# Kernel optimization log

Measured on AMD Instinct MI355X. Metric: run time of the kernel, lower is better.

## Reference

```python
import jax, jax.numpy as jnp
import numpy as np
from jax import lax

# Dense-equivalent of the spconv net: SubMConv/SparseConv with stride 1 and
# size-preserving padding on a dense input reduce to ordinary conv2d.
# Layer chain: (1->64,k1) PReLU (64->256,k3) PReLU (256->512,k3) PReLU
# (512->256,k3) PReLU (256->64,k3) PReLU (64->1,k3) PReLU, then symmetrize.

CHANS = [(1, 64, 1), (64, 256, 3), (256, 512, 3), (512, 256, 3), (256, 64, 3), (64, 1, 3)]


def _conv(x, w, b, k):
    pad = ((k // 2, k // 2), (k // 2, k // 2))
    y = lax.conv_general_dilated(x, w, window_strides=(1, 1), padding=pad,
                                 dimension_numbers=('NCHW', 'OIHW', 'NCHW'))
    return y + b[None, :, None, None]


def _prelu(x, a):
    return jnp.where(x >= 0, x, a * x)


def setup_inputs() -> dict:
    key = jax.random.key(0)
    keys = jax.random.split(key, 1 + 2 * len(CHANS))
    inp = {'A': jax.random.normal(keys[0], (1, 1, 512, 512), dtype=jnp.float32)}
    for i, (cin, cout, k) in enumerate(CHANS):
        fan_in = cin * k * k
        std = 1.0 / np.sqrt(fan_in)
        inp[f'w{i}'] = jax.random.normal(keys[1 + 2 * i], (cout, cin, k, k), dtype=jnp.float32) * std
        inp[f'b{i}'] = jax.random.normal(keys[2 + 2 * i], (cout,), dtype=jnp.float32) * std
        inp[f'p{i}'] = jnp.full((1,), 0.25, dtype=jnp.float32)  # PReLU default weight
    return inp


def reference(A, w0, b0, p0, w1, b1, p1, w2, b2, p2, w3, b3, p3, w4, b4, p4, w5, b5, p5):
    params = [(w0, b0, p0), (w1, b1, p1), (w2, b2, p2), (w3, b3, p3), (w4, b4, p4), (w5, b5, p5)]
    x = A
    for (w, b, p), (_, _, k) in zip(params, CHANS):
        x = _prelu(_conv(x, w, b, k), p)
    # make_symmetric: average with transpose over the spatial (matrix) dims
    return 0.5 * (x + jnp.swapaxes(x, -1, -2))
```

## Files before the change

kernel.cpp:

```cpp
#include <hip/hip_runtime.h>
#include <hip/hip_bf16.h>
#include <stdint.h>

typedef __bf16 bf16_t;
typedef __bf16 bf16x8 __attribute__((ext_vector_type(8)));
typedef float  f32x4  __attribute__((ext_vector_type(4)));

#define HP 514
#define AS1 __attribute__((address_space(1)))
#define AS3 __attribute__((address_space(3)))

__device__ __forceinline__ bf16_t f2bf(float f) { return (bf16_t)f; }

__global__ void l0_kernel(const float* __restrict__ A, const float* __restrict__ w0,
                          const float* __restrict__ b0, const float* __restrict__ p0,
                          bf16_t* __restrict__ X0)
{
    int idx = blockIdx.x * 256 + threadIdx.x;
    if (idx >= HP * HP * 64) return;
    int c   = idx & 63;
    int pix = idx >> 6;
    int py = pix / HP, px = pix - py * HP;
    float v = 0.f;
    if (py >= 1 && py <= 512 && px >= 1 && px <= 512) {
        float a = A[(py - 1) * 512 + (px - 1)];
        v = fmaf(w0[c], a, b0[c]);
        v = v >= 0.f ? v : p0[0] * v;
    }
    X0[idx] = f2bf(v);
}

__global__ void zero_rows_kernel(bf16_t* __restrict__ buf, int C, int r0, int n)
{
    int idx = blockIdx.x * 256 + threadIdx.x;
    int rowsz = HP * C;
    if (idx >= n * rowsz) return;
    int r = idx / rowsz, j = idx - r * rowsz;
    buf[(size_t)(r0 + r) * rowsz + j] = f2bf(0.f);
}

__global__ void zero_cols_kernel(bf16_t* __restrict__ buf, int C, int R)
{
    int idx = blockIdx.x * 256 + threadIdx.x;
    if (idx >= R * 2 * C) return;
    int r = idx / (2 * C);
    int t = idx - r * 2 * C;
    int col = (t < C) ? 0 : 513;
    int c = t % C;
    buf[((size_t)r * HP + col) * C + c] = f2bf(0.f);
}

__global__ void wtrans_kernel(const float* __restrict__ w, bf16_t* __restrict__ wt,
                              int COUT, int CIN)
{
    int idx = blockIdx.x * 256 + threadIdx.x;
    if (idx >= COUT * CIN * 9) return;
    int G    = COUT / 16;
    int j    = idx & 7;
    int l    = (idx >> 3) & 63;
    int t    = idx >> 9;
    int gabs = t % G;
    int t2   = t / G;
    int tap  = t2 % 9;
    int ci   = t2 / 9;
    int cout = gabs * 16 + (l & 15);
    int cin  = ci * 32 + (l >> 4) * 8 + j;
    wt[idx] = f2bf(w[(cout * CIN + cin) * 9 + tap]);
}

template<int CIN, int COUT, int BN>
__global__ __launch_bounds__(256, 2)
void conv3x3_kernel(const bf16_t* __restrict__ in, const bf16_t* __restrict__ wt,
                    const float* __restrict__ bias, const float* __restrict__ alpha,
                    bf16_t* __restrict__ out,
                    int n_rows, int in_off, int in_alloc, int out_off)
{
    constexpr int G      = COUT / 16;
    constexpr int GPB    = BN / 16;
    constexpr int NT     = BN / 32;
    constexpr int NC     = CIN / 32;
    constexpr int AUNITS = 18 * 10 * 4;
    constexpr int ASLAB  = AUNITS * 8;
    constexpr int BSZ    = BN * 32;
    __shared__ __align__(16) bf16_t As[2 * ASLAB];
    __shared__ __align__(16) bf16_t Bs[2 * BSZ];

    const int tid  = threadIdx.x;
    const int lane = tid & 63;
    const int wave = tid >> 6;
    const int lm   = lane & 15;
    const int quad = lane >> 4;
    const int wave_m = wave >> 1;
    const int wave_n = wave & 1;

    const int x0 = blockIdx.x * 8;
    const int y0 = blockIdx.y * 16;
    const int zb = blockIdx.z;
    const int gb_blk = zb * GPB;

    int a_src[3], a_dst[3];
    #pragma unroll
    for (int it = 0; it < 3; ++it) {
        int u  = it * 256 + tid;
        int uu = u < AUNITS ? u : 0;
        int q = uu & 3, px = (uu >> 2) % 10, r = uu / 40;
        int grow = in_off + y0 + r;
        grow = grow < 0 ? 0 : (grow >= in_alloc ? in_alloc - 1 : grow);
        a_src[it] = (grow * HP + x0 + px) * CIN + q * 8;
        a_dst[it] = (r * 40 + px * 4 + ((q + (px >> 1)) & 3)) * 8;
    }

    const int pxb = lm & 7, pyb = lm >> 3;
    int sw[3];
    #pragma unroll
    for (int dx = 0; dx < 3; ++dx)
        sw[dx] = ((quad + ((pxb + dx) >> 1)) & 3) * 8;
    int addrA0[4];
    #pragma unroll
    for (int mt = 0; mt < 4; ++mt)
        addrA0[mt] = ((wave_m * 8 + mt * 2 + pyb) * 40 + pxb * 4) * 8;

    auto loadA = [&](int cc, bf16x8* s) {
        #pragma unroll
        for (int it = 0; it < 3; ++it)
            if (it * 256 + tid < AUNITS)
                s[it] = *(const bf16x8*)(in + a_src[it] + cc);
    };
    auto writeA = [&](const bf16x8* s, int abuf) {
        bf16_t* d = As + abuf * ASLAB;
        #pragma unroll
        for (int it = 0; it < 3; ++it)
            if (it * 256 + tid < AUNITS)
                *(bf16x8*)(d + a_dst[it]) = s[it];
    };
    auto stageB = [&](int ci9t, int bbuf) {
        #pragma unroll
        for (int k = 0; k < GPB / 4; ++k) {
            int g = wave + k * 4;
            const bf16_t* src = wt + ((size_t)ci9t * G + gb_blk + g) * 512 + lane * 8;
            bf16_t* dst = Bs + bbuf * BSZ + g * 512;
            __builtin_amdgcn_global_load_lds((AS1 void*)src, (AS3 void*)dst, 16, 0, 0);
        }
    };

    f32x4 acc[4][NT] = {};
    bf16x8 areg[3];

    loadA(0, areg);
    writeA(areg, 0);
    stageB(0, 0);
    __syncthreads();

    int ab = 0, bb = 0;
    for (int ci = 0; ci < NC; ++ci) {
        const bool more = (ci + 1 < NC);
        #pragma unroll
        for (int tap = 0; tap < 9; ++tap) {
            if (tap < 8)      stageB(ci * 9 + tap + 1, bb ^ 1);
            else if (more)    stageB((ci + 1) * 9, bb ^ 1);
            if (tap == 0 && more) loadA((ci + 1) * 32, areg);

            const int dy = tap / 3, dx = tap - dy * 3;
            const int shift = (dy * 40 + dx * 4) * 8 + sw[dx];
            bf16x8 a[4], b[NT];
            #pragma unroll
            for (int nt = 0; nt < NT; ++nt)
                b[nt] = *(const bf16x8*)(Bs + bb * BSZ + (wave_n * NT + nt) * 512 + lane * 8);
            #pragma unroll
            for (int mt = 0; mt < 4; ++mt)
                a[mt] = *(const bf16x8*)(As + ab * ASLAB + addrA0[mt] + shift);
            #pragma unroll
            for (int mt = 0; mt < 4; ++mt)
                #pragma unroll
                for (int nt = 0; nt < NT; ++nt)
                    acc[mt][nt] = __builtin_amdgcn_mfma_f32_16x16x32_bf16(
                        a[mt], b[nt], acc[mt][nt], 0, 0, 0);

            if (tap == 8 && more) writeA(areg, ab ^ 1);
            __syncthreads();
            bb ^= 1;
        }
        ab ^= 1;
    }

    const float al = alpha[0];
    #pragma unroll
    for (int nt = 0; nt < NT; ++nt) {
        const int n = zb * BN + wave_n * (BN / 2) + nt * 16 + lm;
        const float bv = bias[n];
        #pragma unroll
        for (int mt = 0; mt < 4; ++mt) {
            f32x4 v = acc[mt][nt];
            #pragma unroll
            for (int r = 0; r < 4; ++r) {
                int m  = wave_m * 64 + mt * 16 + quad * 4 + r;
                int py = m >> 3, px = m & 7;
                int ly = y0 + py;
                if (ly < n_rows) {
                    float f = v[r] + bv;
                    f = f >= 0.f ? f : al * f;
                    out[((size_t)(out_off + ly) * HP + (x0 + px + 1)) * COUT + n] = f2bf(f);
                }
            }
        }
    }
}

__device__ __forceinline__ float conv64_at(const bf16_t* __restrict__ X,
                                           const float* __restrict__ wsh,
                                           int y, int x, float bv)
{
    float acc = bv;
    #pragma unroll
    for (int dy = 0; dy < 3; ++dy) {
        #pragma unroll
        for (int dx = 0; dx < 3; ++dx) {
            const bf16x8* p = (const bf16x8*)(X + ((size_t)(y + dy) * HP + (x + dx)) * 64);
            const float* wf = wsh + (dy * 3 + dx) * 64;
            #pragma unroll
            for (int j = 0; j < 8; ++j) {
                bf16x8 v = p[j];
                #pragma unroll
                for (int k = 0; k < 8; ++k)
                    acc = fmaf((float)v[k], wf[j * 8 + k], acc);
            }
        }
    }
    return acc;
}

__global__ __launch_bounds__(256)
void l5_strip_kernel(const bf16_t* __restrict__ B4, const bf16_t* __restrict__ wt5,
                     const float* __restrict__ b5, const float* __restrict__ p5,
                     float* __restrict__ T, int abs_row0)
{
    __shared__ float wsh[9 * 64];
    for (int i = threadIdx.x; i < 576; i += 256) wsh[i] = (float)wt5[i];
    __syncthreads();
    int idx = blockIdx.x * 256 + threadIdx.x;
    int ly = idx >> 9, x = idx & 511;
    float bv = b5[0], al = p5[0];
    float t = conv64_at(B4, wsh, ly, x, bv);
    t = t >= 0.f ? t : al * t;
    T[(size_t)(abs_row0 + ly) * 512 + x] = t;
}

__global__ void wtrans5_kernel(const float* __restrict__ w, bf16_t* __restrict__ wt)
{
    int idx = blockIdx.x * 256 + threadIdx.x;
    if (idx >= 9 * 64) return;
    int cin = idx % 64, tap = idx / 64;
    wt[idx] = f2bf(w[cin * 9 + tap]);
}

__global__ __launch_bounds__(256)
void sym_kernel(const float* __restrict__ T, float* __restrict__ out)
{
    int idx = blockIdx.x * 256 + threadIdx.x;
    int y = idx >> 9, x = idx & 511;
    out[idx] = 0.5f * (T[idx] + T[x * 512 + y]);
}

extern "C" void kernel_launch(void* const* d_in, const int* in_sizes, int n_in,
                              void* d_out, int out_size, void* d_ws, size_t ws_size,
                              hipStream_t stream)
{
    const float* A = (const float*)d_in[0];
    const float *w[6], *b[6], *p[6];
    for (int i = 0; i < 6; ++i) {
        w[i] = (const float*)d_in[1 + 3 * i];
        b[i] = (const float*)d_in[2 + 3 * i];
        p[i] = (const float*)d_in[3 + 3 * i];
    }

    auto footprint = [](long long S) -> size_t {
        auto al = [](size_t v) { return (v + 255) & ~(size_t)255; };
        size_t t = 0;
        t += al((size_t)HP * HP * 64 * 2);
        t += al((size_t)(S + 8) * HP * 256 * 2);
        t += al((size_t)(S + 6) * HP * 512 * 2);
        t += al((size_t)(S + 2) * HP * 64 * 2);
        t += al((size_t)512 * 512 * 4);
        t += al((size_t)9 * 256 * 64 * 2);
        t += al((size_t)9 * 512 * 256 * 2);
        t += al((size_t)9 * 256 * 512 * 2);
        t += al((size_t)9 * 64 * 256 * 2);
        t += al((size_t)9 * 64 * 2);
        return t;
    };
    const int cand[6] = {512, 256, 128, 64, 32, 16};
    int S = 16;
    for (int i = 0; i < 6; ++i)
        if (footprint(cand[i]) <= ws_size) { S = cand[i]; break; }
    const int nStrips = 512 / S;

    char* ws = (char*)d_ws;
    size_t off = 0;
    auto carve = [&](size_t bytes) -> void* {
        void* r = ws + off;
        off += (bytes + 255) & ~(size_t)255;
        return r;
    };
    bf16_t* X0  = (bf16_t*)carve((size_t)HP * HP * 64 * 2);
    bf16_t* B1  = (bf16_t*)carve((size_t)(S + 8) * HP * 256 * 2);
    bf16_t* B2  = (bf16_t*)carve((size_t)(S + 6) * HP * 512 * 2);
    bf16_t* B4  = (bf16_t*)carve((size_t)(S + 2) * HP * 64 * 2);
    float*  T   = (float*)carve((size_t)512 * 512 * 4);
    bf16_t* wt1 = (bf16_t*)carve((size_t)9 * 256 * 64 * 2);
    bf16_t* wt2 = (bf16_t*)carve((size_t)9 * 512 * 256 * 2);
    bf16_t* wt3 = (bf16_t*)carve((size_t)9 * 256 * 512 * 2);
    bf16_t* wt4 = (bf16_t*)carve((size_t)9 * 64 * 256 * 2);
    bf16_t* wt5 = (bf16_t*)carve((size_t)9 * 64 * 2);
    bf16_t* B3  = B1;

    auto cdiv = [](int a, int bq) { return (a + bq - 1) / bq; };
    auto zrows = [&](bf16_t* buf, int C, int r0, int n) {
        if (n > 0)
            zero_rows_kernel<<<cdiv(n * HP * C, 256), 256, 0, stream>>>(buf, C, r0, n);
    };

    wtrans_kernel<<<cdiv(9 * 256 * 64, 256), 256, 0, stream>>>(w[1], wt1, 256, 64);
    wtrans_kernel<<<cdiv(9 * 512 * 256, 256), 256, 0, stream>>>(w[2], wt2, 512, 256);
    wtrans_kernel<<<cdiv(9 * 256 * 512, 256), 256, 0, stream>>>(w[3], wt3, 256, 512);
    wtrans_kernel<<<cdiv(9 * 64 * 256, 256), 256, 0, stream>>>(w[4], wt4, 64, 256);
    wtrans5_kernel<<<cdiv(9 * 64, 256), 256, 0, stream>>>(w[5], wt5);
    l0_kernel<<<cdiv(HP * HP * 64, 256), 256, 0, stream>>>(A, w[0], b[0], p[0], X0);
    zero_cols_kernel<<<cdiv((S + 8) * 2 * 256, 256), 256, 0, stream>>>(B1, 256, S + 8);
    zero_cols_kernel<<<cdiv((S + 6) * 2 * 512, 256), 256, 0, stream>>>(B2, 512, S + 6);
    zero_cols_kernel<<<cdiv((S + 2) * 2 * 64, 256), 256, 0, stream>>>(B4, 64, S + 2);

    for (int s = 0; s < nStrips; ++s) {
        const int base = S * s;
        int o0[5], nn[5], ooff[5], alloc[5];
        for (int k = 1; k <= 4; ++k) {
            int hk = 5 - k;
            int a0 = base - hk, a1 = base + S + hk;
            int c0 = a0 < 0 ? 0 : a0, c1 = a1 > 512 ? 512 : a1;
            o0[k] = c0; nn[k] = c1 - c0; ooff[k] = c0 - a0; alloc[k] = S + 2 * hk;
        }
        {
            int in_off = o0[1];
            dim3 g(64, cdiv(nn[1], 16), 2);
            conv3x3_kernel<64, 256, 128><<<g, 256, 0, stream>>>(
                X0, wt1, b[1], p[1], B1, nn[1], in_off, 514, ooff[1]);
            zrows(B1, 256, 0, ooff[1]);
            zrows(B1, 256, ooff[1] + nn[1], alloc[1] - ooff[1] - nn[1]);
        }
        {
            int in_off = (o0[2] - 1) - (base - 4);
            dim3 g(64, cdiv(nn[2], 16), 4);
            conv3x3_kernel<256, 512, 128><<<g, 256, 0, stream>>>(
                B1, wt2, b[2], p[2], B2, nn[2], in_off, alloc[1], ooff[2]);
            zrows(B2, 512, 0, ooff[2]);
            zrows(B2, 512, ooff[2] + nn[2], alloc[2] - ooff[2] - nn[2]);
        }
        {
            int in_off = (o0[3] - 1) - (base - 3);
            dim3 g(64, cdiv(nn[3], 16), 2);
            conv3x3_kernel<512, 256, 128><<<g, 256, 0, stream>>>(
                B2, wt3, b[3], p[3], B3, nn[3], in_off, alloc[2], ooff[3]);
            zrows(B3, 256, 0, ooff[3]);
            zrows(B3, 256, ooff[3] + nn[3], alloc[3] - ooff[3] - nn[3]);
        }
        {
            int in_off = (o0[4] - 1) - (base - 2);
            dim3 g(64, cdiv(nn[4], 16), 1);
            conv3x3_kernel<256, 64, 64><<<g, 256, 0, stream>>>(
                B3, wt4, b[4], p[4], B4, nn[4], in_off, alloc[3], ooff[4]);
            zrows(B4, 64, 0, ooff[4]);
            zrows(B4, 64, ooff[4] + nn[4], alloc[4] - ooff[4] - nn[4]);
        }
        l5_strip_kernel<<<(S * 512) / 256, 256, 0, stream>>>(B4, wt5, b[5], p[5], T, base);
    }

    sym_kernel<<<(512 * 512) / 256, 256, 0, stream>>>(T, (float*)d_out);
}
```

Measured before the change: 1.597 ms.

## Process two filter taps per barrier with doubled B staging buffers

The main conv loop now walks channel chunks in pairs and handles two tap slices of weights per pipeline step. It stages both slices into a doubled B LDS buffer, which halves the number of __syncthreads barriers and pipeline steps. A-tile loads and writes are rescheduled so the two A buffers hold consecutive channel chunks. The cost is more LDS for B, which may lower occupancy, and the change assumes an even number of channel chunks.

```diff
diff --git a/kernel.cpp b/kernel.cpp
--- a/kernel.cpp
+++ b/kernel.cpp
@@ -83,7 +83,7 @@
     constexpr int ASLAB  = AUNITS * 8;
     constexpr int BSZ    = BN * 32;
     __shared__ __align__(16) bf16_t As[2 * ASLAB];
-    __shared__ __align__(16) bf16_t Bs[2 * BSZ];
+    __shared__ __align__(16) bf16_t Bs[2 * 2 * BSZ];
 
     const int tid  = threadIdx.x;
     const int lane = tid & 63;
@@ -133,12 +133,12 @@
             if (it * 256 + tid < AUNITS)
                 *(bf16x8*)(d + a_dst[it]) = s[it];
     };
-    auto stageB = [&](int ci9t, int bbuf) {
+    auto stageB = [&](int ft, int bbuf, int sub) {
         #pragma unroll
         for (int k = 0; k < GPB / 4; ++k) {
             int g = wave + k * 4;
-            const bf16_t* src = wt + ((size_t)ci9t * G + gb_blk + g) * 512 + lane * 8;
-            bf16_t* dst = Bs + bbuf * BSZ + g * 512;
+            const bf16_t* src = wt + ((size_t)ft * G + gb_blk + g) * 512 + lane * 8;
+            bf16_t* dst = Bs + (bbuf * 2 + sub) * BSZ + g * 512;
             __builtin_amdgcn_global_load_lds((AS1 void*)src, (AS3 void*)dst, 16, 0, 0);
         }
     };
@@ -148,39 +148,51 @@
 
     loadA(0, areg);
     writeA(areg, 0);
-    stageB(0, 0);
+    stageB(0, 0, 0);
+    stageB(1, 0, 1);
     __syncthreads();
 
-    int ab = 0, bb = 0;
-    for (int ci = 0; ci < NC; ++ci) {
-        const bool more = (ci + 1 < NC);
-        #pragma unroll
-        for (int tap = 0; tap < 9; ++tap) {
-            if (tap < 8)      stageB(ci * 9 + tap + 1, bb ^ 1);
-            else if (more)    stageB((ci + 1) * 9, bb ^ 1);
-            if (tap == 0 && more) loadA((ci + 1) * 32, areg);
-
-            const int dy = tap / 3, dx = tap - dy * 3;
-            const int shift = (dy * 40 + dx * 4) * 8 + sw[dx];
-            bf16x8 a[4], b[NT];
+    int bb = 0;
+    for (int cp = 0; cp < NC / 2; ++cp) {
+        const bool more = (cp + 1 < NC / 2);
+        #pragma unroll
+        for (int q = 0; q < 9; ++q) {
+            const int nf = 18 * cp + 2 * q + 2;
+            if (q < 8 || more) {
+                stageB(nf,     bb ^ 1, 0);
+                stageB(nf + 1, bb ^ 1, 1);
+            }
             #pragma unroll
-            for (int nt = 0; nt < NT; ++nt)
-                b[nt] = *(const bf16x8*)(Bs + bb * BSZ + (wave_n * NT + nt) * 512 + lane * 8);
-            #pragma unroll
-            for (int mt = 0; mt < 4; ++mt)
-                a[mt] = *(const bf16x8*)(As + ab * ASLAB + addrA0[mt] + shift);
-            #pragma unroll
-            for (int mt = 0; mt < 4; ++mt)
+            for (int sub = 0; sub < 2; ++sub) {
+                const int rf  = 2 * q + sub;
+                const int ab  = rf >= 9 ? 1 : 0;
+                const int tap = rf - 9 * ab;
+
+                if (rf == 0)          loadA((2 * cp + 1) * 32, areg);
+                if (rf == 9 && more)  loadA((2 * cp + 2) * 32, areg);
+                if (rf == 4)          writeA(areg, 1);
+                if (rf == 13 && more) writeA(areg, 0);
+
+                const int dy = tap / 3, dx = tap - dy * 3;
+                const int shift = (dy * 40 + dx * 4) * 8 + sw[dx];
+                bf16x8 a[4], b[NT];
                 #pragma unroll
                 for (int nt = 0; nt < NT; ++nt)
-                    acc[mt][nt] = __builtin_amdgcn_mfma_f32_16x16x32_bf16(
-                        a[mt], b[nt], acc[mt][nt], 0, 0, 0);
-
-            if (tap == 8 && more) writeA(areg, ab ^ 1);
+                    b[nt] = *(const bf16x8*)(Bs + (bb * 2 + sub) * BSZ +
+                                             (wave_n * NT + nt) * 512 + lane * 8);
+                #pragma unroll
+                for (int mt = 0; mt < 4; ++mt)
+                    a[mt] = *(const bf16x8*)(As + ab * ASLAB + addrA0[mt] + shift);
+                #pragma unroll
+                for (int mt = 0; mt < 4; ++mt)
+                    #pragma unroll
+                    for (int nt = 0; nt < NT; ++nt)
+                        acc[mt][nt] = __builtin_amdgcn_mfma_f32_16x16x32_bf16(
+                            a[mt], b[nt], acc[mt][nt], 0, 0, 0);
+            }
             __syncthreads();
             bb ^= 1;
         }
-        ab ^= 1;
     }
 
     const float al = alpha[0];
```

After: 1.734 ms. 8.6% more time.

## Load conv weights straight to registers and stage activations via async LDS loads

Applied to the files above, without the earlier changes.

Weight fragments are no longer staged through shared memory. Each wave now loads its B fragments directly from global memory into double-buffered registers, one tap ahead. The activation tile now goes to LDS through global_load_lds, with the swizzle moved to the source address. The loop handles two input-channel chunks per iteration, so barriers drop from one per tap to one per nine taps. The cost is more register pressure and redundant global weight loads across the waves that share the same columns, which are served by L2.

```diff
diff --git a/kernel.cpp b/kernel.cpp
--- a/kernel.cpp
+++ b/kernel.cpp
@@ -76,14 +76,12 @@
                     int n_rows, int in_off, int in_alloc, int out_off)
 {
     constexpr int G      = COUT / 16;
-    constexpr int GPB    = BN / 16;
     constexpr int NT     = BN / 32;
     constexpr int NC     = CIN / 32;
     constexpr int AUNITS = 18 * 10 * 4;
-    constexpr int ASLAB  = AUNITS * 8;
-    constexpr int BSZ    = BN * 32;
+    constexpr int APAD   = 768;
+    constexpr int ASLAB  = APAD * 8;
     __shared__ __align__(16) bf16_t As[2 * ASLAB];
-    __shared__ __align__(16) bf16_t Bs[2 * BSZ];
 
     const int tid  = threadIdx.x;
     const int lane = tid & 63;
@@ -96,18 +94,18 @@
     const int x0 = blockIdx.x * 8;
     const int y0 = blockIdx.y * 16;
     const int zb = blockIdx.z;
-    const int gb_blk = zb * GPB;
-
-    int a_src[3], a_dst[3];
+    const int gb_blk = zb * (BN / 16);
+
+    int a_srcb[3];
     #pragma unroll
     for (int it = 0; it < 3; ++it) {
         int u  = it * 256 + tid;
-        int uu = u < AUNITS ? u : 0;
-        int q = uu & 3, px = (uu >> 2) % 10, r = uu / 40;
+        int uu = u < AUNITS ? u : AUNITS - 1;
+        int qq = uu & 3, px = (uu >> 2) % 10, r = uu / 40;
+        int q  = (qq - (px >> 1)) & 3;
         int grow = in_off + y0 + r;
         grow = grow < 0 ? 0 : (grow >= in_alloc ? in_alloc - 1 : grow);
-        a_src[it] = (grow * HP + x0 + px) * CIN + q * 8;
-        a_dst[it] = (r * 40 + px * 4 + ((q + (px >> 1)) & 3)) * 8;
+        a_srcb[it] = (grow * HP + x0 + px) * CIN + q * 8;
     }
 
     const int pxb = lm & 7, pyb = lm >> 3;
@@ -120,52 +118,43 @@
     for (int mt = 0; mt < 4; ++mt)
         addrA0[mt] = ((wave_m * 8 + mt * 2 + pyb) * 40 + pxb * 4) * 8;
 
-    auto loadA = [&](int cc, bf16x8* s) {
-        #pragma unroll
-        for (int it = 0; it < 3; ++it)
-            if (it * 256 + tid < AUNITS)
-                s[it] = *(const bf16x8*)(in + a_src[it] + cc);
-    };
-    auto writeA = [&](const bf16x8* s, int abuf) {
-        bf16_t* d = As + abuf * ASLAB;
-        #pragma unroll
-        for (int it = 0; it < 3; ++it)
-            if (it * 256 + tid < AUNITS)
-                *(bf16x8*)(d + a_dst[it]) = s[it];
-    };
-    auto stageB = [&](int ci9t, int bbuf) {
-        #pragma unroll
-        for (int k = 0; k < GPB / 4; ++k) {
-            int g = wave + k * 4;
-            const bf16_t* src = wt + ((size_t)ci9t * G + gb_blk + g) * 512 + lane * 8;
-            bf16_t* dst = Bs + bbuf * BSZ + g * 512;
+    auto stageA = [&](int cc, int abuf) {
+        #pragma unroll
+        for (int it = 0; it < 3; ++it) {
+            const bf16_t* src = in + a_srcb[it] + cc;
+            bf16_t* dst = As + abuf * ASLAB + (it * 256 + wave * 64) * 8;
             __builtin_amdgcn_global_load_lds((AS1 void*)src, (AS3 void*)dst, 16, 0, 0);
         }
     };
+    auto loadB = [&](int ft, bf16x8* b) {
+        const bf16_t* base = wt + ((size_t)ft * G + gb_blk + wave_n * NT) * 512 + lane * 8;
+        #pragma unroll
+        for (int nt = 0; nt < NT; ++nt)
+            b[nt] = *(const bf16x8*)(base + nt * 512);
+    };
 
     f32x4 acc[4][NT] = {};
-    bf16x8 areg[3];
-
-    loadA(0, areg);
-    writeA(areg, 0);
-    stageB(0, 0);
+    bf16x8 breg[2][NT];
+
+    stageA(0, 0);
+    loadB(0, breg[0]);
     __syncthreads();
 
-    int ab = 0, bb = 0;
-    for (int ci = 0; ci < NC; ++ci) {
-        const bool more = (ci + 1 < NC);
-        #pragma unroll
-        for (int tap = 0; tap < 9; ++tap) {
-            if (tap < 8)      stageB(ci * 9 + tap + 1, bb ^ 1);
-            else if (more)    stageB((ci + 1) * 9, bb ^ 1);
-            if (tap == 0 && more) loadA((ci + 1) * 32, areg);
-
+    for (int cp = 0; cp < NC / 2; ++cp) {
+        const bool morecp = (cp + 1 < NC / 2);
+        const int fb = cp * 18;
+        #pragma unroll
+        for (int rf = 0; rf < 18; ++rf) {
+            if (rf < 17 || morecp)
+                loadB(fb + rf + 1, breg[(rf + 1) & 1]);
+            if (rf == 0)            stageA((2 * cp + 1) * 32, 1);
+            if (rf == 9 && morecp)  stageA((2 * cp + 2) * 32, 0);
+
+            const int ab  = (rf >= 9);
+            const int tap = rf % 9;
             const int dy = tap / 3, dx = tap - dy * 3;
             const int shift = (dy * 40 + dx * 4) * 8 + sw[dx];
-            bf16x8 a[4], b[NT];
-            #pragma unroll
-            for (int nt = 0; nt < NT; ++nt)
-                b[nt] = *(const bf16x8*)(Bs + bb * BSZ + (wave_n * NT + nt) * 512 + lane * 8);
+            bf16x8 a[4];
             #pragma unroll
             for (int mt = 0; mt < 4; ++mt)
                 a[mt] = *(const bf16x8*)(As + ab * ASLAB + addrA0[mt] + shift);
@@ -174,13 +163,10 @@
                 #pragma unroll
                 for (int nt = 0; nt < NT; ++nt)
                     acc[mt][nt] = __builtin_amdgcn_mfma_f32_16x16x32_bf16(
-                        a[mt], b[nt], acc[mt][nt], 0, 0, 0);
-
-            if (tap == 8 && more) writeA(areg, ab ^ 1);
-            __syncthreads();
-            bb ^= 1;
-        }
-        ab ^= 1;
+                        a[mt], breg[rf & 1][nt], acc[mt][nt], 0, 0, 0);
+
+            if (rf == 8 || (rf == 17 && morecp)) __syncthreads();
+        }
     }
 
     const float al = alpha[0];
```

Result: no change. 1.583 ms (-0.9%).
